# Optimization experiments

Measured on AMD Instinct MI355X. Metric: run time of the kernel, lower is better.

## Reference

```python
import jax, jax.numpy as jnp
import numpy as np
from jax.scipy.linalg import solve_triangular
from jax.scipy.special import logsumexp

N, T, M, K = 16384, 60, 8, 2


def setup_inputs() -> dict:
    key = jax.random.key(0)
    k1, k2, k3, k4 = jax.random.split(key, 4)
    mu = jax.random.normal(k1, (N, T, M, K), dtype=jnp.float32)
    # Build SPD covariance: sigma = A A^T + 0.5 I (module runs cholesky on it)
    A = 0.3 * jax.random.normal(k2, (N, T, M, K, K), dtype=jnp.float32)
    sigma = A @ jnp.swapaxes(A, -1, -2) + 0.5 * jnp.eye(K, dtype=jnp.float32)
    pi = jax.random.normal(k3, (N, M), dtype=jnp.float32)
    x = jax.random.normal(k4, (N, T, K), dtype=jnp.float32)
    mask = jnp.ones((N, T), dtype=jnp.float32)
    return {"mu": mu, "sigma": sigma, "pi": pi, "x": x, "mask": mask}


def reference(mu, sigma, pi, x, mask):
    k = mu.shape[-1]
    LOG_2PI = 1.8378770664093453
    # batched small-matrix Cholesky: (N,T,m,k,k)
    L = jnp.linalg.cholesky(sigma)
    diff = x[:, :, None, :] - mu                       # (N,T,m,k)
    # triangular solve L z = diff -> Mahalanobis term
    z = solve_triangular(L, diff[..., None], lower=True)[..., 0]
    maha = jnp.sum(z * z, axis=-1)                     # (N,T,m)
    log_det = jnp.sum(jnp.log(jnp.diagonal(L, axis1=-2, axis2=-1)), axis=-1)
    mvn_lp = -0.5 * (k * LOG_2PI + maha) - log_det     # (N,T,m)
    # Categorical(logits=pi) -> normalized log-probs, broadcast over T
    log_pi = jax.nn.log_softmax(pi, axis=-1)[:, None, :]  # (N,1,m)
    gmm_lp = logsumexp(log_pi + mvn_lp, axis=-1)       # (N,T)
    comp_loss = -gmm_lp
    # mask_reduce_losses: per-timestep mean over valid batch entries, then sum
    n_pred = jnp.sum(mask, axis=0)                     # (T,)
    t_losses = jnp.sum(comp_loss * mask, axis=0) / n_pred
    return jnp.sum(t_losses)
```

## Files before the change

kernel.cpp:

```cpp
#include <hip/hip_runtime.h>

#define T_DIM 60
#define NBLK 3840

typedef float v4f __attribute__((ext_vector_type(4)));
typedef float v2f __attribute__((ext_vector_type(2)));

__global__ __launch_bounds__(256, 8)
void loss_fused_kernel(const float* __restrict__ mu,
                       const float* __restrict__ sigma,
                       const float* __restrict__ pi,
                       const float* __restrict__ x,
                       const float* __restrict__ mask,
                       float* __restrict__ loss_p,
                       float* __restrict__ mask_p,
                       float* __restrict__ out) {
    __shared__ float bl[T_DIM], bm[T_DIM];
    __shared__ float s_lsepi[8];
    __shared__ float s_piv[48];
    __shared__ v2f   s_x[256];
    __shared__ float s_mk[256];
    const float LOG_2PI = 1.8378770664093453f;
    int tid = threadIdx.x;
    int E0 = blockIdx.x * 256;
    int n_base = E0 / T_DIM;
    int ncnt = (E0 + 255) / T_DIM - n_base + 1;

    if (tid < T_DIM) { bl[tid] = 0.0f; bm[tid] = 0.0f; }
    s_x[tid]  = ((const v2f*)x)[E0 + tid];
    s_mk[tid] = mask[E0 + tid];
    if (tid < 8 * ncnt)
        s_piv[tid] = pi[(size_t)n_base * 8 + tid] - LOG_2PI;
    if (tid < ncnt) {
        const float* pr = pi + (size_t)(n_base + tid) * 8;
        float q0 = pr[0], q1 = pr[1], q2 = pr[2], q3 = pr[3];
        float q4 = pr[4], q5 = pr[5], q6 = pr[6], q7 = pr[7];
        float mx = fmaxf(fmaxf(fmaxf(q0, q1), fmaxf(q2, q3)),
                         fmaxf(fmaxf(q4, q5), fmaxf(q6, q7)));
        float s = __expf(q0 - mx) + __expf(q1 - mx) + __expf(q2 - mx) +
                  __expf(q3 - mx) + __expf(q4 - mx) + __expf(q5 - mx) +
                  __expf(q6 - mx) + __expf(q7 - mx);
        s_lsepi[tid] = mx + __logf(s);
    }
    if (blockIdx.x == 0 && tid == 0) out[0] = 0.0f;
    __syncthreads();

    int l = tid & 7;
    int oct = tid >> 3;
    int e = E0 + oct;
    int idx = oct;
    int n0 = e / T_DIM;
    int t = e - n0 * T_DIM;
    int nb = n0 - n_base;

#pragma unroll
    for (int it = 0; it < 8; ++it) {
        v4f sg = ((const v4f*)sigma)[(size_t)e * 8 + l];
        v2f m2 = ((const v2f*)mu)[(size_t)e * 8 + l];
        v2f xv = s_x[idx];
        float mk = s_mk[idx];
        float pv = s_piv[nb * 8 + l];

        float a = sg.x, b = sg.y, c = sg.w;
        float d1 = xv.x - m2.x, d2 = xv.y - m2.y;
        float det = a * c - b * b;
        float rdet = __builtin_amdgcn_rcpf(det);
        float maha = (c * d1 * d1 - 2.0f * b * d1 * d2 + a * d2 * d2) * rdet;
        float g = __expf(__builtin_fmaf(-0.5f, maha, pv)) *
                  __builtin_amdgcn_rsqf(det);

        float s = g;
        s += __shfl_xor(s, 1);
        s += __shfl_xor(s, 2);
        s += __shfl_xor(s, 4);

        if (l == 0) {
            float v = (s_lsepi[nb] - __logf(s)) * mk;
            atomicAdd(&bl[t], v);
            atomicAdd(&bm[t], mk);
        }

        e += 32;
        idx += 32;
        t += 32;
        if (t >= T_DIM) { t -= T_DIM; nb += 1; }
    }
    __syncthreads();
    if (tid < T_DIM) {
        loss_p[(size_t)tid * NBLK + blockIdx.x] = bl[tid];
        mask_p[(size_t)tid * NBLK + blockIdx.x] = bm[tid];
    }
}

__global__ void reduce_t_kernel(const float* __restrict__ loss_p,
                                const float* __restrict__ mask_p,
                                float* __restrict__ out, int nblocks) {
    int t = blockIdx.x;
    const float* lrow = loss_p + (size_t)t * nblocks;
    const float* mrow = mask_p + (size_t)t * nblocks;
    float sl = 0.0f, sm = 0.0f;
    for (int i = threadIdx.x; i < nblocks; i += blockDim.x) {
        sl += lrow[i]; sm += mrow[i];
    }
#pragma unroll
    for (int off = 32; off > 0; off >>= 1) {
        sl += __shfl_down(sl, off); sm += __shfl_down(sm, off);
    }
    __shared__ float wl[4], wm[4];
    int lane = threadIdx.x & 63, w = threadIdx.x >> 6;
    if (lane == 0) { wl[w] = sl; wm[w] = sm; }
    __syncthreads();
    if (threadIdx.x == 0)
        atomicAdd(out, (wl[0] + wl[1] + wl[2] + wl[3]) /
                       (wm[0] + wm[1] + wm[2] + wm[3]));
}

extern "C" void kernel_launch(void* const* d_in, const int* in_sizes, int n_in,
                              void* d_out, int out_size, void* d_ws, size_t ws_size,
                              hipStream_t stream) {
    const float* mu    = (const float*)d_in[0];
    const float* sigma = (const float*)d_in[1];
    const float* pi    = (const float*)d_in[2];
    const float* x     = (const float*)d_in[3];
    const float* mask  = (const float*)d_in[4];
    float* out = (float*)d_out;
    float* ws = (float*)d_ws;
    float* loss_p = ws;
    float* mask_p = ws + (size_t)T_DIM * NBLK;

    hipLaunchKernelGGL(loss_fused_kernel, dim3(NBLK), dim3(256), 0, stream,
                       mu, sigma, pi, x, mask, loss_p, mask_p, out);
    hipLaunchKernelGGL(reduce_t_kernel, dim3(T_DIM), dim3(256), 0, stream,
                       loss_p, mask_p, out, NBLK);
}
```

Measured before the change: 243.0 us.

## Stage sigma and mu tiles into LDS via async global_load_lds

Each block now issues direct global-to-LDS loads for its whole tile of sigma (32KB) and mu (16KB) at kernel start, overlapping with the pi/x/mask setup, then reads from LDS in the compute loop. The element mapping is changed so each wave processes a contiguous 64-element chunk that matches its own LDS region. The min-blocks launch bound is dropped. This targets load latency and transaction efficiency, but about 50KB of LDS per block sharply limits occupancy on a memory-bound kernel.

```diff
diff --git a/kernel.cpp b/kernel.cpp
--- a/kernel.cpp
+++ b/kernel.cpp
@@ -6,7 +6,10 @@
 typedef float v4f __attribute__((ext_vector_type(4)));
 typedef float v2f __attribute__((ext_vector_type(2)));
 
-__global__ __launch_bounds__(256, 8)
+typedef const unsigned __attribute__((address_space(1)))* gptr_t;
+typedef unsigned __attribute__((address_space(3)))* lptr_t;
+
+__global__ __launch_bounds__(256)
 void loss_fused_kernel(const float* __restrict__ mu,
                        const float* __restrict__ sigma,
                        const float* __restrict__ pi,
@@ -15,6 +18,8 @@
                        float* __restrict__ loss_p,
                        float* __restrict__ mask_p,
                        float* __restrict__ out) {
+    __shared__ v4f   s_sig[2048];
+    __shared__ v2f   s_mu[2048];
     __shared__ float bl[T_DIM], bm[T_DIM];
     __shared__ float s_lsepi[8];
     __shared__ float s_piv[48];
@@ -25,6 +30,21 @@
     int E0 = blockIdx.x * 256;
     int n_base = E0 / T_DIM;
     int ncnt = (E0 + 255) / T_DIM - n_base + 1;
+
+    int lane = tid & 63;
+    int w    = tid >> 6;
+    const char* gs = (const char*)sigma + (size_t)E0 * 128 + (size_t)w * 8192 + (size_t)lane * 16;
+    const char* gm = (const char*)mu    + (size_t)E0 * 64  + (size_t)w * 4096 + (size_t)lane * 16;
+    char* ls = (char*)s_sig + w * 8192;
+    char* lm = (char*)s_mu  + w * 4096;
+#pragma unroll
+    for (int g = 0; g < 8; ++g)
+        __builtin_amdgcn_global_load_lds((gptr_t)(gs + g * 1024),
+                                         (lptr_t)(ls + g * 1024), 16, 0, 0);
+#pragma unroll
+    for (int g = 0; g < 4; ++g)
+        __builtin_amdgcn_global_load_lds((gptr_t)(gm + g * 1024),
+                                         (lptr_t)(lm + g * 1024), 16, 0, 0);
 
     if (tid < T_DIM) { bl[tid] = 0.0f; bm[tid] = 0.0f; }
     s_x[tid]  = ((const v2f*)x)[E0 + tid];
@@ -45,20 +65,21 @@
     if (blockIdx.x == 0 && tid == 0) out[0] = 0.0f;
     __syncthreads();
 
-    int l = tid & 7;
-    int oct = tid >> 3;
-    int e = E0 + oct;
-    int idx = oct;
-    int n0 = e / T_DIM;
-    int t = e - n0 * T_DIM;
+    int l  = tid & 7;
+    int oc = (tid >> 3) & 7;
+    int w512 = w * 512;
+    int bidx = w * 64 + oc;
+    int e0w  = E0 + bidx;
+    int n0 = e0w / T_DIM;
+    int t  = e0w - n0 * T_DIM;
     int nb = n0 - n_base;
 
 #pragma unroll
     for (int it = 0; it < 8; ++it) {
-        v4f sg = ((const v4f*)sigma)[(size_t)e * 8 + l];
-        v2f m2 = ((const v2f*)mu)[(size_t)e * 8 + l];
-        v2f xv = s_x[idx];
-        float mk = s_mk[idx];
+        v4f sg = s_sig[w512 + (it * 8 + oc) * 8 + l];
+        v2f m2 = s_mu [w512 + (it * 8 + oc) * 8 + l];
+        v2f xv = s_x[bidx];
+        float mk = s_mk[bidx];
         float pv = s_piv[nb * 8 + l];
 
         float a = sg.x, b = sg.y, c = sg.w;
@@ -66,10 +87,10 @@
         float det = a * c - b * b;
         float rdet = __builtin_amdgcn_rcpf(det);
         float maha = (c * d1 * d1 - 2.0f * b * d1 * d2 + a * d2 * d2) * rdet;
-        float g = __expf(__builtin_fmaf(-0.5f, maha, pv)) *
-                  __builtin_amdgcn_rsqf(det);
+        float g2 = __expf(__builtin_fmaf(-0.5f, maha, pv)) *
+                   __builtin_amdgcn_rsqf(det);
 
-        float s = g;
+        float s = g2;
         s += __shfl_xor(s, 1);
         s += __shfl_xor(s, 2);
         s += __shfl_xor(s, 4);
@@ -80,11 +101,11 @@
             atomicAdd(&bm[t], mk);
         }
 
-        e += 32;
-        idx += 32;
-        t += 32;
+        bidx += 8;
+        t += 8;
         if (t >= T_DIM) { t -= T_DIM; nb += 1; }
     }
+
     __syncthreads();
     if (tid < T_DIM) {
         loss_p[(size_t)tid * NBLK + blockIdx.x] = bl[tid];
```

New measurement: 247.9 us. 1.02x slower.
